# Kernel optimization log

Measured on AMD Instinct MI355X. Metric: run time of the kernel, lower is better.

The kernel has to match this reference:

```python
import jax, jax.numpy as jnp
import numpy as np

B, S, D, H = 2, 2048, 2048, 16
HD = D // H


def setup_inputs() -> dict:
    key = jax.random.key(0)
    ks = jax.random.split(key, 11)
    scale = 1.0 / np.sqrt(D)
    causal = jnp.tril(jnp.ones((S, S), dtype=bool))
    attention_mask = jnp.broadcast_to(causal, (B, H, S, S))
    return {
        "queries": jax.random.normal(ks[0], (B, S, D), dtype=jnp.float32),
        "keys": jax.random.normal(ks[1], (B, S, D), dtype=jnp.float32),
        "values": jax.random.normal(ks[2], (B, S, D), dtype=jnp.float32),
        "attention_mask": attention_mask,
        "wq": jax.random.normal(ks[3], (D, D), dtype=jnp.float32) * scale,
        "bq": jax.random.normal(ks[4], (D,), dtype=jnp.float32) * 0.01,
        "wk": jax.random.normal(ks[5], (D, D), dtype=jnp.float32) * scale,
        "bk": jax.random.normal(ks[6], (D,), dtype=jnp.float32) * 0.01,
        "wv": jax.random.normal(ks[7], (D, D), dtype=jnp.float32) * scale,
        "bv": jax.random.normal(ks[8], (D,), dtype=jnp.float32) * 0.01,
        "wo": jax.random.normal(ks[9], (D, D), dtype=jnp.float32) * scale,
        "bo": jax.random.normal(ks[10], (D,), dtype=jnp.float32) * 0.01,
    }


def _split_heads(x):
    # (B, S, D) -> (B, H, S, HD)
    b, s, _ = x.shape
    return x.reshape(b, s, H, HD).transpose(0, 2, 1, 3)


def reference(queries, keys, values, attention_mask, wq, bq, wk, bk, wv, bv, wo, bo):
    # Linear layers (torch convention: x @ W.T + b)
    q = _split_heads(queries @ wq.T + bq)   # (B, H, S, HD)
    k = _split_heads(keys @ wk.T + bk)
    v = _split_heads(values @ wv.T + bv)

    inv_sqrt_d = 1.0 / jnp.sqrt(jnp.asarray(HD, dtype=q.dtype))
    scores = jnp.einsum('bhqd,bhkd->bhqk', q, k) * inv_sqrt_d  # (B, H, S, S)
    scores = jnp.where(attention_mask, scores, jnp.asarray(-jnp.inf, dtype=scores.dtype))
    probs = jax.nn.softmax(scores, axis=-1)
    out = jnp.einsum('bhqk,bhkd->bhqd', probs, v)              # (B, H, S, HD)

    out = out.transpose(0, 2, 1, 3).reshape(queries.shape[0], queries.shape[1], D)
    return out @ wo.T + bo
```

## Files before the change

### kernel.cpp

```cpp
#include <hip/hip_runtime.h>
#include <hip/hip_bf16.h>

typedef unsigned short u16;
typedef __bf16 bf16x8 __attribute__((ext_vector_type(8)));
typedef short  short8 __attribute__((ext_vector_type(8)));
typedef float  f32x4  __attribute__((ext_vector_type(4)));
typedef u16    u16x4  __attribute__((ext_vector_type(4)));

#define BB 2
#define SS 2048
#define DD 2048
#define HH 16
#define HDIM 128
#define MM (BB * SS)
#define KSCALE 0.12752039505554602f

static __device__ __forceinline__ f32x4 mfma16(short8 a, short8 b, f32x4 c) {
    return __builtin_amdgcn_mfma_f32_16x16x32_bf16(
        __builtin_bit_cast(bf16x8, a), __builtin_bit_cast(bf16x8, b), c, 0, 0, 0);
}

static __device__ __forceinline__ u16 f2bf(float f) {
    union { float f; unsigned u; } v; v.f = f;
    unsigned r = v.u + 0x7fffu + ((v.u >> 16) & 1u);
    return (u16)(r >> 16);
}

static __device__ __forceinline__ float bf2f(u16 v) {
    union { unsigned u; float f; } t; t.u = ((unsigned)v) << 16;
    return t.f;
}

static __device__ __forceinline__ uint4 pack8(float4 a, float4 b) {
    uint4 o;
    o.x = (unsigned)f2bf(a.x) | ((unsigned)f2bf(a.y) << 16);
    o.y = (unsigned)f2bf(a.z) | ((unsigned)f2bf(a.w) << 16);
    o.z = (unsigned)f2bf(b.x) | ((unsigned)f2bf(b.y) << 16);
    o.w = (unsigned)f2bf(b.z) | ((unsigned)f2bf(b.w) << 16);
    return o;
}

static __device__ __forceinline__ void gload_lds16(const u16* g, u16* l) {
    __builtin_amdgcn_global_load_lds(
        (const __attribute__((address_space(1))) unsigned int*)g,
        (__attribute__((address_space(3))) unsigned int*)l, 16, 0, 0);
}

__global__ __launch_bounds__(256) void conv_all(
    const float* __restrict__ q, const float* __restrict__ k, const float* __restrict__ v,
    const float* __restrict__ wq, const float* __restrict__ wk,
    const float* __restrict__ wv, const float* __restrict__ wo,
    u16* __restrict__ out)
{
    constexpr int n1 = MM * DD / 8;
    constexpr int nw = DD * DD / 8;
    constexpr int total = 3 * n1 + 4 * nw;
    const int stride = gridDim.x * blockDim.x;
    for (int i = blockIdx.x * blockDim.x + threadIdx.x; i < total; i += stride) {
        const float* s; int j = i; float sc = 1.f;
        if (j < n1)            { s = q; }
        else if (j < 2 * n1)   { s = k;  j -= n1; }
        else if (j < 3 * n1)   { s = v;  j -= 2 * n1; }
        else {
            j -= 3 * n1;
            if (j < nw)        { s = wq; sc = KSCALE; }
            else if (j < 2*nw) { s = wk; j -= nw; }
            else if (j < 3*nw) { s = wv; j -= 2 * nw; }
            else               { s = wo; j -= 3 * nw; }
        }
        const float4* sp = (const float4*)s + (size_t)j * 2;
        float4 a = sp[0], bb2 = sp[1];
        a.x *= sc; a.y *= sc; a.z *= sc; a.w *= sc;
        bb2.x *= sc; bb2.y *= sc; bb2.z *= sc; bb2.w *= sc;
        ((uint4*)out)[i] = pack8(a, bb2);
    }
}

__global__ __launch_bounds__(256, 3) void gemm_qkv(
    const u16* __restrict__ A0, const u16* __restrict__ W0,
    const float* __restrict__ bq, const float* __restrict__ bk,
    const float* __restrict__ bv, u16* __restrict__ C0)
{
    __shared__ u16 S[128 * 132];
    u16* Al = S;
    u16* Bl = S + 4096;

    const int z = blockIdx.z;
    const u16* A  = A0 + (size_t)z * MM * DD;
    const u16* Wb = W0 + (size_t)z * DD * DD;
    const float* bias = (z == 0) ? bq : (z == 1 ? bk : bv);
    const float bsc = (z == 0) ? KSCALE : 1.f;

    const int tid = threadIdx.x;
    const int lane = tid & 63;
    const int lg = lane >> 4, li = lane & 15;
    const int wid = tid >> 6;
    const int brow = blockIdx.x * 128, bcol = blockIdx.y * 128;
    const int wm = wid >> 1, wn = wid & 1;

    const int srow = tid >> 2;
    const int scol = (tid & 3) * 8;

    const f32x4 zero = {0.f, 0.f, 0.f, 0.f};
    f32x4 acc[4][4];
#pragma unroll
    for (int i = 0; i < 4; ++i)
#pragma unroll
        for (int j = 0; j < 4; ++j) acc[i][j] = zero;

    const u16* aptr = A  + (size_t)(brow + srow) * DD + scol;
    const u16* bptr = Wb + (size_t)(bcol + srow) * DD + scol;
    const size_t half = (size_t)64 * DD;

    for (int kt = 0; kt < DD; kt += 32) {
        gload_lds16(aptr + kt,        &Al[tid * 8]);
        gload_lds16(aptr + half + kt, &Al[2048 + tid * 8]);
        gload_lds16(bptr + kt,        &Bl[tid * 8]);
        gload_lds16(bptr + half + kt, &Bl[2048 + tid * 8]);
        __syncthreads();

        short8 af[4], bf[4];
#pragma unroll
        for (int mi = 0; mi < 4; ++mi)
            af[mi] = *(const short8*)(&Al[(wm * 64 + mi * 16 + li) * 32 + lg * 8]);
#pragma unroll
        for (int ni = 0; ni < 4; ++ni)
            bf[ni] = *(const short8*)(&Bl[(wn * 64 + ni * 16 + li) * 32 + lg * 8]);
#pragma unroll
        for (int mi = 0; mi < 4; ++mi)
#pragma unroll
            for (int ni = 0; ni < 4; ++ni)
                acc[mi][ni] = mfma16(af[mi], bf[ni], acc[mi][ni]);
        __syncthreads();
    }

    if (z == 2) {
        u16* Cl = S;
#pragma unroll
        for (int ni = 0; ni < 4; ++ni) {
            const int cc = wn * 64 + ni * 16 + li;
            const float bvv = bias[bcol + cc];
#pragma unroll
            for (int mi = 0; mi < 4; ++mi)
#pragma unroll
                for (int r = 0; r < 4; ++r) {
                    const int rr = wm * 64 + mi * 16 + lg * 4 + r;
                    Cl[cc * 132 + rr] = f2bf(acc[mi][ni][r] + bvv);
                }
        }
        __syncthreads();
        const int row = tid >> 1;
        const int hcol = (tid & 1) * 64;
        u16* dst = C0 + (size_t)2 * MM * DD + (size_t)(bcol + row) * MM + brow + hcol;
#pragma unroll
        for (int c = 0; c < 8; ++c)
            *(short8*)(dst + c * 8) = *(const short8*)(&Cl[row * 132 + hcol + c * 8]);
    } else {
        u16* Cp = C0 + (size_t)z * MM * DD;
#pragma unroll
        for (int ni = 0; ni < 4; ++ni) {
            const int col = bcol + wn * 64 + ni * 16 + li;
            const float bvv = bias[col] * bsc;
#pragma unroll
            for (int mi = 0; mi < 4; ++mi)
#pragma unroll
                for (int r = 0; r < 4; ++r) {
                    const int row = brow + wm * 64 + mi * 16 + lg * 4 + r;
                    Cp[(size_t)row * DD + col] = f2bf(acc[mi][ni][r] + bvv);
                }
        }
    }
}

__global__ __launch_bounds__(256) void gemm_out(
    const u16* __restrict__ A, const u16* __restrict__ Wb,
    const float* __restrict__ bias, float* __restrict__ Cp)
{
    __shared__ u16 Al[128 * 32];
    __shared__ u16 Bl[128 * 32];

    const int tid = threadIdx.x;
    const int lane = tid & 63;
    const int lg = lane >> 4, li = lane & 15;
    const int wid = tid >> 6;
    const int brow = blockIdx.x * 128, bcol = blockIdx.y * 128;
    const int wm = wid >> 1, wn = wid & 1;

    const int srow = tid >> 2;
    const int scol = (tid & 3) * 8;

    const f32x4 zero = {0.f, 0.f, 0.f, 0.f};
    f32x4 acc[4][4];
#pragma unroll
    for (int i = 0; i < 4; ++i)
#pragma unroll
        for (int j = 0; j < 4; ++j) acc[i][j] = zero;

    const u16* aptr = A  + (size_t)(brow + srow) * DD + scol;
    const u16* bptr = Wb + (size_t)(bcol + srow) * DD + scol;
    const size_t half = (size_t)64 * DD;

    for (int kt = 0; kt < DD; kt += 32) {
        gload_lds16(aptr + kt,        &Al[tid * 8]);
        gload_lds16(aptr + half + kt, &Al[2048 + tid * 8]);
        gload_lds16(bptr + kt,        &Bl[tid * 8]);
        gload_lds16(bptr + half + kt, &Bl[2048 + tid * 8]);
        __syncthreads();

        short8 af[4], bf[4];
#pragma unroll
        for (int mi = 0; mi < 4; ++mi)
            af[mi] = *(const short8*)(&Al[(wm * 64 + mi * 16 + li) * 32 + lg * 8]);
#pragma unroll
        for (int ni = 0; ni < 4; ++ni)
            bf[ni] = *(const short8*)(&Bl[(wn * 64 + ni * 16 + li) * 32 + lg * 8]);
#pragma unroll
        for (int mi = 0; mi < 4; ++mi)
#pragma unroll
            for (int ni = 0; ni < 4; ++ni)
                acc[mi][ni] = mfma16(af[mi], bf[ni], acc[mi][ni]);
        __syncthreads();
    }

#pragma unroll
    for (int ni = 0; ni < 4; ++ni) {
        const int col = bcol + wn * 64 + ni * 16 + li;
        const float bvv = bias[col];
#pragma unroll
        for (int mi = 0; mi < 4; ++mi)
#pragma unroll
            for (int r = 0; r < 4; ++r) {
                const int row = brow + wm * 64 + mi * 16 + lg * 4 + r;
                Cp[(size_t)row * DD + col] = acc[mi][ni][r] + bvv;
            }
    }
}

__global__ __launch_bounds__(256) void flash_attn(
    const u16* __restrict__ Q, const u16* __restrict__ Kp,
    const u16* __restrict__ Vt, u16* __restrict__ O,
    u16* __restrict__ PartO, float* __restrict__ PartML)
{
    constexpr int SP = 72;
    __shared__ u16 lds[16384 + 4 * 32 * SP];
    u16* Kl = lds;
    u16* Vl = lds + 8192;
    u16* Pl = lds + 16384;

    const int tid = threadIdx.x;
    const int wid = tid >> 6, lane = tid & 63;
    const int lg = lane >> 4, li = lane & 15;
    const int h = blockIdx.y, b = blockIdx.z;

    const int f = 39 - (int)blockIdx.x;
    int qt, ch;
    if (f < 4)       { qt = f;               ch = 0; }
    else if (f < 12) { int g = f - 4;  qt = 4  + (g >> 1); ch = g & 1; }
    else if (f < 24) { int g = f - 12; qt = 8  + g / 3;    ch = g % 3; }
    else             { int g = f - 24; qt = 12 + (g >> 2); ch = g & 3; }
    const int j0 = ch * 8;
    const int j1 = min(j0 + 8, 2 * qt + 2);
    const int qbase = qt * 128 + wid * 32;

    const int rK0 = tid >> 4, wK0 = tid & 15;
    const int bK0 = ((wK0 * 16) ^ ((rK0 & 7) << 4)) >> 1;
    const int rV0 = tid >> 3, wV0 = tid & 7;
    const int bV0 = ((wV0 * 16) ^ ((rV0 & 7) << 4)) >> 1;
    const u16* kbase = Kp + (size_t)(b * SS + rK0) * DD + h * HDIM + bK0;
    const u16* vbase = Vt + (size_t)(h * HDIM + rV0) * MM + b * SS + bV0;

    short8 qf[4][2];
    {
        const u16* qp0 = Q + (size_t)(b * SS + qbase + li) * DD + h * HDIM + lg * 8;
#pragma unroll
        for (int qh = 0; qh < 2; ++qh)
#pragma unroll
            for (int s = 0; s < 4; ++s)
                qf[s][qh] = *(const short8*)(qp0 + (size_t)qh * 16 * DD + s * 32);
    }

    const f32x4 zero = {0.f, 0.f, 0.f, 0.f};
    float m_r[2], l_r[2];
    m_r[0] = m_r[1] = -__builtin_inff();
    l_r[0] = l_r[1] = 0.f;
    f32x4 accO[8][2];
#pragma unroll
    for (int d = 0; d < 8; ++d) accO[d][0] = accO[d][1] = zero;

    for (int j = j0; j < j1; ++j) {
#pragma unroll
        for (int i_ = 0; i_ < 4; ++i_) {
            gload_lds16(kbase + (size_t)(j * 64 + i_ * 16) * DD, &Kl[(i_ * 256 + tid) * 8]);
            gload_lds16(vbase + (size_t)(i_ * 32) * MM + j * 64, &Vl[(i_ * 256 + tid) * 8]);
        }
        __syncthreads();

        if (j * 64 <= qbase + 31) {
            f32x4 accS[4][2];
#pragma unroll
            for (int nb = 0; nb < 4; ++nb) accS[nb][0] = accS[nb][1] = zero;
            __builtin_amdgcn_s_setprio(1);
#pragma unroll
            for (int s = 0; s < 4; ++s) {
#pragma unroll
                for (int nb = 0; nb < 4; ++nb) {
                    const int R = nb * 16 + li;
                    const int e = ((s * 64 + lg * 16) ^ ((R & 7) << 4)) >> 1;
                    short8 kf = *(const short8*)(&Kl[R * 128 + e]);
#pragma unroll
                    for (int qh = 0; qh < 2; ++qh)
                        accS[nb][qh] = mfma16(kf, qf[s][qh], accS[nb][qh]);
                }
            }
            __builtin_amdgcn_s_setprio(0);

            const bool domask = (j * 64 + 63 > qbase);
            float rmax[2];
            rmax[0] = rmax[1] = -__builtin_inff();
#pragma unroll
            for (int nb = 0; nb < 4; ++nb)
#pragma unroll
                for (int qh = 0; qh < 2; ++qh)
#pragma unroll
                    for (int r = 0; r < 4; ++r) {
                        float t = accS[nb][qh][r];
                        if (domask && (j * 64 + nb * 16 + lg * 4 + r >
                                       qbase + qh * 16 + li)) t = -__builtin_inff();
                        accS[nb][qh][r] = t;
                        rmax[qh] = fmaxf(rmax[qh], t);
                    }
#pragma unroll
            for (int qh = 0; qh < 2; ++qh) {
                rmax[qh] = fmaxf(rmax[qh], __shfl_xor(rmax[qh], 16, 64));
                rmax[qh] = fmaxf(rmax[qh], __shfl_xor(rmax[qh], 32, 64));
            }

            const bool need = (rmax[0] - m_r[0] > 11.5f) || (rmax[1] - m_r[1] > 11.5f);
            if (__any(need)) {
#pragma unroll
                for (int qh = 0; qh < 2; ++qh) {
                    const float mn = fmaxf(m_r[qh], rmax[qh]);
                    const float sf = exp2f(m_r[qh] - mn);
                    m_r[qh] = mn;
                    l_r[qh] *= sf;
#pragma unroll
                    for (int mb = 0; mb < 8; ++mb)
#pragma unroll
                        for (int r = 0; r < 4; ++r) accO[mb][qh][r] *= sf;
                }
            }

            float ls[2] = {0.f, 0.f};
#pragma unroll
            for (int nb = 0; nb < 4; ++nb)
#pragma unroll
                for (int qh = 0; qh < 2; ++qh)
#pragma unroll
                    for (int r = 0; r < 4; ++r) {
                        const float e = exp2f(accS[nb][qh][r] - m_r[qh]);
                        accS[nb][qh][r] = e;
                        ls[qh] += e;
                    }
#pragma unroll
            for (int qh = 0; qh < 2; ++qh) {
                ls[qh] += __shfl_xor(ls[qh], 16, 64);
                ls[qh] += __shfl_xor(ls[qh], 32, 64);
                l_r[qh] += ls[qh];
            }

#pragma unroll
            for (int nb = 0; nb < 4; ++nb)
#pragma unroll
                for (int qh = 0; qh < 2; ++qh) {
                    u16x4 pk;
                    pk.x = f2bf(accS[nb][qh][0]);
                    pk.y = f2bf(accS[nb][qh][1]);
                    pk.z = f2bf(accS[nb][qh][2]);
                    pk.w = f2bf(accS[nb][qh][3]);
                    *(u16x4*)(&Pl[(wid * 32 + qh * 16 + li) * SP + nb * 16 + lg * 4]) = pk;
                }

            __builtin_amdgcn_s_setprio(1);
#pragma unroll
            for (int s2 = 0; s2 < 2; ++s2) {
                short8 pf[2];
#pragma unroll
                for (int qh = 0; qh < 2; ++qh)
                    pf[qh] = *(const short8*)(&Pl[(wid * 32 + qh * 16 + li) * SP +
                                                  s2 * 32 + lg * 8]);
#pragma unroll
                for (int mb = 0; mb < 8; ++mb) {
                    const int R2 = mb * 16 + li;
                    const int e2 = ((s2 * 64 + lg * 16) ^ ((R2 & 7) << 4)) >> 1;
                    short8 vf = *(const short8*)(&Vl[R2 * 64 + e2]);
#pragma unroll
                    for (int qh = 0; qh < 2; ++qh)
                        accO[mb][qh] = mfma16(vf, pf[qh], accO[mb][qh]);
                }
            }
            __builtin_amdgcn_s_setprio(0);
        }
        __syncthreads();
    }

    if (f >= 4) {
        const int pslot = (b * HH + h) * 36 + (f - 4);
        u16* po = PartO + (size_t)pslot * 16384;
#pragma unroll
        for (int mb = 0; mb < 8; ++mb)
#pragma unroll
            for (int qh = 0; qh < 2; ++qh) {
                const int q_g = wid * 32 + qh * 16 + li;
#pragma unroll
                for (int r = 0; r < 4; ++r) {
                    const int d = mb * 16 + lg * 4 + r;
                    po[d * 128 + q_g] = f2bf(accO[mb][qh][r]);
                }
            }
        if (lg == 0) {
            float* ml = PartML + (size_t)pslot * 256;
#pragma unroll
            for (int qh = 0; qh < 2; ++qh) {
                ml[wid * 32 + qh * 16 + li]       = m_r[qh];
                ml[128 + wid * 32 + qh * 16 + li] = l_r[qh];
            }
        }
    } else {
        float linv[2] = {1.f / l_r[0], 1.f / l_r[1]};
        u16* Wl = lds + wid * 4096;
#pragma unroll
        for (int mb = 0; mb < 8; ++mb)
#pragma unroll
            for (int qh = 0; qh < 2; ++qh) {
                const int q_l = qh * 16 + li;
                const int dbase = mb * 16 + lg * 4;
                u16x4 pk;
                pk.x = f2bf(accO[mb][qh][0] * linv[qh]);
                pk.y = f2bf(accO[mb][qh][1] * linv[qh]);
                pk.z = f2bf(accO[mb][qh][2] * linv[qh]);
                pk.w = f2bf(accO[mb][qh][3] * linv[qh]);
                *(u16x4*)(&Wl[q_l * 128 + (dbase ^ ((q_l & 7) << 4))]) = pk;
            }
        const int q_l = lane >> 1;
        const int d0 = (lane & 1) * 64;
        u16* op = O + (size_t)(b * SS + qt * 128 + wid * 32 + q_l) * DD + h * HDIM + d0;
#pragma unroll
        for (int c = 0; c < 8; ++c) {
            short8 vv = *(const short8*)(&Wl[q_l * 128 + ((d0 + c * 8) ^ ((q_l & 7) << 4))]);
            *(short8*)(op + c * 8) = vv;
        }
    }
}

__global__ __launch_bounds__(256) void attn_combine(
    const u16* __restrict__ PartO, const float* __restrict__ PartML,
    u16* __restrict__ O)
{
    const int qt = 4 + (int)blockIdx.x;
    const int h = blockIdx.y, b = blockIdx.z;
    const int nch = qt / 4 + 1;
    int f0m4;
    if (qt < 8)       f0m4 = (qt - 4) * 2;
    else if (qt < 12) f0m4 = 8 + (qt - 8) * 3;
    else              f0m4 = 20 + (qt - 12) * 4;
    const int pbase = (b * HH + h) * 36 + f0m4;

    const int tid = threadIdx.x;
    const int q = tid & 127;
    const int d0 = (tid >> 7) * 64;

    float mc[4], lc[4];
#pragma unroll
    for (int c = 0; c < 4; ++c) {
        if (c < nch) {
            mc[c] = PartML[(size_t)(pbase + c) * 256 + q];
            lc[c] = PartML[(size_t)(pbase + c) * 256 + 128 + q];
        } else { mc[c] = -__builtin_inff(); lc[c] = 0.f; }
    }
    float M = fmaxf(fmaxf(mc[0], mc[1]), fmaxf(mc[2], mc[3]));
    float wc[4], L = 0.f;
#pragma unroll
    for (int c = 0; c < 4; ++c) { wc[c] = exp2f(mc[c] - M); L += wc[c] * lc[c]; }
    const float Linv = 1.f / L;

    float acc[64];
#pragma unroll
    for (int i = 0; i < 64; ++i) acc[i] = 0.f;
#pragma unroll
    for (int c = 0; c < 4; ++c) {
        if (c < nch) {
            const float w = wc[c] * Linv;
            const u16* po = PartO + (size_t)(pbase + c) * 16384 + q;
#pragma unroll
            for (int i = 0; i < 64; ++i)
                acc[i] += w * bf2f(po[(size_t)(d0 + i) * 128]);
        }
    }

    u16* op = O + (size_t)(b * SS + qt * 128 + q) * DD + h * HDIM + d0;
#pragma unroll
    for (int j = 0; j < 8; ++j) {
        short8 vv;
#pragma unroll
        for (int e = 0; e < 8; ++e) vv[e] = (short)f2bf(acc[j * 8 + e]);
        *(short8*)(op + j * 8) = vv;
    }
}

extern "C" void kernel_launch(void* const* d_in, const int* in_sizes, int n_in,
                              void* d_out, int out_size, void* d_ws, size_t ws_size,
                              hipStream_t stream)
{
    const float* queries = (const float*)d_in[0];
    const float* keys    = (const float*)d_in[1];
    const float* values  = (const float*)d_in[2];
    const float* wq = (const float*)d_in[4];
    const float* bq = (const float*)d_in[5];
    const float* wk = (const float*)d_in[6];
    const float* bk = (const float*)d_in[7];
    const float* wv = (const float*)d_in[8];
    const float* bv = (const float*)d_in[9];
    const float* wo = (const float*)d_in[10];
    const float* bo = (const float*)d_in[11];

    const int NMD = MM * DD;
    const int NWW = DD * DD;

    u16* qb  = (u16*)d_ws;
    u16* wqb = qb  + (size_t)3 * NMD;
    u16* wob = wqb + (size_t)3 * NWW;
    u16* qw  = wob + (size_t)NWW;
    u16* aw  = qw  + (size_t)3 * NMD;
    u16*   partO  = qb;
    float* partML = (float*)wqb;
    (void)in_sizes; (void)n_in; (void)out_size; (void)ws_size;

    dim3 blk(256);
    dim3 gridC(2048);
    dim3 gridQKV(MM / 128, DD / 128, 3);
    dim3 gridO(MM / 128, DD / 128);
    dim3 gridA(40, HH, BB);
    dim3 gridX(12, HH, BB);

    conv_all<<<gridC, blk, 0, stream>>>(queries, keys, values, wq, wk, wv, wo, qb);
    gemm_qkv<<<gridQKV, blk, 0, stream>>>(qb, wqb, bq, bk, bv, qw);
    flash_attn<<<gridA, blk, 0, stream>>>(qw, qw + (size_t)NMD, qw + (size_t)2 * NMD, aw,
                                          partO, partML);
    attn_combine<<<gridX, blk, 0, stream>>>(partO, partML, aw);
    gemm_out<<<gridO, blk, 0, stream>>>(aw, wob, bo, (float*)d_out);
}
```

Measured before the change: 349.1 us.

## Switch flash attention to 32x32x16 MFMA with single-row-per-lane softmax

Rewrites the attention inner loops to use 32x32x16 bf16 MFMA instead of 16x16x32, so each lane owns a single query row. Row max and sum reductions need one cross-lane shuffle instead of two, fewer LDS fragment loads are issued per MFMA, and per-row softmax state shrinks to scalars. The partial-output layout changes from d-major to q-major so writes are vectorized, and the combine kernel reads contiguous elements to match. Risks include different register pressure, possible LDS bank conflicts from the new swizzle indexing, and correctness of the new C-fragment mapping.

```diff
diff --git a/kernel.cpp b/kernel.cpp
--- a/kernel.cpp
+++ b/kernel.cpp
@@ -5,6 +5,7 @@
 typedef __bf16 bf16x8 __attribute__((ext_vector_type(8)));
 typedef short  short8 __attribute__((ext_vector_type(8)));
 typedef float  f32x4  __attribute__((ext_vector_type(4)));
+typedef float  f32x16 __attribute__((ext_vector_type(16)));
 typedef u16    u16x4  __attribute__((ext_vector_type(4)));
 
 #define BB 2
@@ -17,6 +18,11 @@
 
 static __device__ __forceinline__ f32x4 mfma16(short8 a, short8 b, f32x4 c) {
     return __builtin_amdgcn_mfma_f32_16x16x32_bf16(
+        __builtin_bit_cast(bf16x8, a), __builtin_bit_cast(bf16x8, b), c, 0, 0, 0);
+}
+
+static __device__ __forceinline__ f32x16 mfma32(short8 a, short8 b, f32x16 c) {
+    return __builtin_amdgcn_mfma_f32_32x32x16_bf16(
         __builtin_bit_cast(bf16x8, a), __builtin_bit_cast(bf16x8, b), c, 0, 0, 0);
 }
 
@@ -249,7 +255,8 @@
 
     const int tid = threadIdx.x;
     const int wid = tid >> 6, lane = tid & 63;
-    const int lg = lane >> 4, li = lane & 15;
+    const int l5 = lane & 31;
+    const int hi = lane >> 5;
     const int h = blockIdx.y, b = blockIdx.z;
 
     const int f = 39 - (int)blockIdx.x;
@@ -261,6 +268,7 @@
     const int j0 = ch * 8;
     const int j1 = min(j0 + 8, 2 * qt + 2);
     const int qbase = qt * 128 + wid * 32;
+    const int qg = qbase + l5;
 
     const int rK0 = tid >> 4, wK0 = tid & 15;
     const int bK0 = ((wK0 * 16) ^ ((rK0 & 7) << 4)) >> 1;
@@ -269,23 +277,18 @@
     const u16* kbase = Kp + (size_t)(b * SS + rK0) * DD + h * HDIM + bK0;
     const u16* vbase = Vt + (size_t)(h * HDIM + rV0) * MM + b * SS + bV0;
 
-    short8 qf[4][2];
+    short8 qf[8];
     {
-        const u16* qp0 = Q + (size_t)(b * SS + qbase + li) * DD + h * HDIM + lg * 8;
-#pragma unroll
-        for (int qh = 0; qh < 2; ++qh)
-#pragma unroll
-            for (int s = 0; s < 4; ++s)
-                qf[s][qh] = *(const short8*)(qp0 + (size_t)qh * 16 * DD + s * 32);
-    }
-
-    const f32x4 zero = {0.f, 0.f, 0.f, 0.f};
-    float m_r[2], l_r[2];
-    m_r[0] = m_r[1] = -__builtin_inff();
-    l_r[0] = l_r[1] = 0.f;
-    f32x4 accO[8][2];
-#pragma unroll
-    for (int d = 0; d < 8; ++d) accO[d][0] = accO[d][1] = zero;
+        const u16* qp0 = Q + (size_t)(b * SS + qg) * DD + h * HDIM + hi * 8;
+#pragma unroll
+        for (int ks = 0; ks < 8; ++ks)
+            qf[ks] = *(const short8*)(qp0 + ks * 16);
+    }
+
+    float m_r = -__builtin_inff(), l_r = 0.f;
+    f32x16 accO[4];
+#pragma unroll
+    for (int d = 0; d < 4; ++d) accO[d] = (f32x16)(0.f);
 
     for (int j = j0; j < j1; ++j) {
 #pragma unroll
@@ -296,106 +299,78 @@
         __syncthreads();
 
         if (j * 64 <= qbase + 31) {
-            f32x4 accS[4][2];
-#pragma unroll
-            for (int nb = 0; nb < 4; ++nb) accS[nb][0] = accS[nb][1] = zero;
+            f32x16 accS[2];
+            accS[0] = (f32x16)(0.f); accS[1] = (f32x16)(0.f);
             __builtin_amdgcn_s_setprio(1);
 #pragma unroll
-            for (int s = 0; s < 4; ++s) {
-#pragma unroll
-                for (int nb = 0; nb < 4; ++nb) {
-                    const int R = nb * 16 + li;
-                    const int e = ((s * 64 + lg * 16) ^ ((R & 7) << 4)) >> 1;
-                    short8 kf = *(const short8*)(&Kl[R * 128 + e]);
-#pragma unroll
-                    for (int qh = 0; qh < 2; ++qh)
-                        accS[nb][qh] = mfma16(kf, qf[s][qh], accS[nb][qh]);
+            for (int ks = 0; ks < 8; ++ks) {
+#pragma unroll
+                for (int kvb = 0; kvb < 2; ++kvb) {
+                    const int row = kvb * 32 + l5;
+                    const int e = (ks * 16 + hi * 8) ^ ((row & 7) << 3);
+                    short8 kf = *(const short8*)(&Kl[row * 128 + e]);
+                    accS[kvb] = mfma32(kf, qf[ks], accS[kvb]);
                 }
             }
             __builtin_amdgcn_s_setprio(0);
 
             const bool domask = (j * 64 + 63 > qbase);
-            float rmax[2];
-            rmax[0] = rmax[1] = -__builtin_inff();
-#pragma unroll
-            for (int nb = 0; nb < 4; ++nb)
-#pragma unroll
-                for (int qh = 0; qh < 2; ++qh)
-#pragma unroll
-                    for (int r = 0; r < 4; ++r) {
-                        float t = accS[nb][qh][r];
-                        if (domask && (j * 64 + nb * 16 + lg * 4 + r >
-                                       qbase + qh * 16 + li)) t = -__builtin_inff();
-                        accS[nb][qh][r] = t;
-                        rmax[qh] = fmaxf(rmax[qh], t);
-                    }
-#pragma unroll
-            for (int qh = 0; qh < 2; ++qh) {
-                rmax[qh] = fmaxf(rmax[qh], __shfl_xor(rmax[qh], 16, 64));
-                rmax[qh] = fmaxf(rmax[qh], __shfl_xor(rmax[qh], 32, 64));
+            float rmax = -__builtin_inff();
+#pragma unroll
+            for (int kvb = 0; kvb < 2; ++kvb)
+#pragma unroll
+                for (int r = 0; r < 16; ++r) {
+                    float t = accS[kvb][r];
+                    const int kv = j * 64 + kvb * 32 + (r & 3) + 8 * (r >> 2) + 4 * hi;
+                    if (domask && kv > qg) t = -__builtin_inff();
+                    accS[kvb][r] = t;
+                    rmax = fmaxf(rmax, t);
+                }
+            rmax = fmaxf(rmax, __shfl_xor(rmax, 32, 64));
+
+            if (!__all(rmax - m_r <= 11.5f)) {
+                const float mn = fmaxf(m_r, rmax);
+                const float sf = exp2f(m_r - mn);
+                m_r = mn;
+                l_r *= sf;
+#pragma unroll
+                for (int db = 0; db < 4; ++db) accO[db] = accO[db] * sf;
             }
 
-            const bool need = (rmax[0] - m_r[0] > 11.5f) || (rmax[1] - m_r[1] > 11.5f);
-            if (__any(need)) {
-#pragma unroll
-                for (int qh = 0; qh < 2; ++qh) {
-                    const float mn = fmaxf(m_r[qh], rmax[qh]);
-                    const float sf = exp2f(m_r[qh] - mn);
-                    m_r[qh] = mn;
-                    l_r[qh] *= sf;
-#pragma unroll
-                    for (int mb = 0; mb < 8; ++mb)
-#pragma unroll
-                        for (int r = 0; r < 4; ++r) accO[mb][qh][r] *= sf;
-                }
-            }
-
-            float ls[2] = {0.f, 0.f};
-#pragma unroll
-            for (int nb = 0; nb < 4; ++nb)
-#pragma unroll
-                for (int qh = 0; qh < 2; ++qh)
-#pragma unroll
-                    for (int r = 0; r < 4; ++r) {
-                        const float e = exp2f(accS[nb][qh][r] - m_r[qh]);
-                        accS[nb][qh][r] = e;
-                        ls[qh] += e;
-                    }
-#pragma unroll
-            for (int qh = 0; qh < 2; ++qh) {
-                ls[qh] += __shfl_xor(ls[qh], 16, 64);
-                ls[qh] += __shfl_xor(ls[qh], 32, 64);
-                l_r[qh] += ls[qh];
-            }
-
-#pragma unroll
-            for (int nb = 0; nb < 4; ++nb)
-#pragma unroll
-                for (int qh = 0; qh < 2; ++qh) {
+            float ls = 0.f;
+#pragma unroll
+            for (int kvb = 0; kvb < 2; ++kvb)
+#pragma unroll
+                for (int r = 0; r < 16; ++r) {
+                    const float e = exp2f(accS[kvb][r] - m_r);
+                    accS[kvb][r] = e;
+                    ls += e;
+                }
+            ls += __shfl_xor(ls, 32, 64);
+            l_r += ls;
+
+#pragma unroll
+            for (int kvb = 0; kvb < 2; ++kvb)
+#pragma unroll
+                for (int g = 0; g < 4; ++g) {
                     u16x4 pk;
-                    pk.x = f2bf(accS[nb][qh][0]);
-                    pk.y = f2bf(accS[nb][qh][1]);
-                    pk.z = f2bf(accS[nb][qh][2]);
-                    pk.w = f2bf(accS[nb][qh][3]);
-                    *(u16x4*)(&Pl[(wid * 32 + qh * 16 + li) * SP + nb * 16 + lg * 4]) = pk;
+                    pk.x = f2bf(accS[kvb][g * 4 + 0]);
+                    pk.y = f2bf(accS[kvb][g * 4 + 1]);
+                    pk.z = f2bf(accS[kvb][g * 4 + 2]);
+                    pk.w = f2bf(accS[kvb][g * 4 + 3]);
+                    *(u16x4*)(&Pl[(wid * 32 + l5) * SP + kvb * 32 + g * 8 + hi * 4]) = pk;
                 }
 
             __builtin_amdgcn_s_setprio(1);
 #pragma unroll
-            for (int s2 = 0; s2 < 2; ++s2) {
-                short8 pf[2];
-#pragma unroll
-                for (int qh = 0; qh < 2; ++qh)
-                    pf[qh] = *(const short8*)(&Pl[(wid * 32 + qh * 16 + li) * SP +
-                                                  s2 * 32 + lg * 8]);
-#pragma unroll
-                for (int mb = 0; mb < 8; ++mb) {
-                    const int R2 = mb * 16 + li;
-                    const int e2 = ((s2 * 64 + lg * 16) ^ ((R2 & 7) << 4)) >> 1;
-                    short8 vf = *(const short8*)(&Vl[R2 * 64 + e2]);
-#pragma unroll
-                    for (int qh = 0; qh < 2; ++qh)
-                        accO[mb][qh] = mfma16(vf, pf[qh], accO[mb][qh]);
+            for (int ks = 0; ks < 4; ++ks) {
+                short8 pf = *(const short8*)(&Pl[(wid * 32 + l5) * SP + ks * 16 + hi * 8]);
+#pragma unroll
+                for (int db = 0; db < 4; ++db) {
+                    const int row = db * 32 + l5;
+                    const int e = (ks * 16 + hi * 8) ^ ((row & 7) << 3);
+                    short8 vf = *(const short8*)(&Vl[row * 64 + e]);
+                    accO[db] = mfma32(vf, pf, accO[db]);
                 }
             }
             __builtin_amdgcn_s_setprio(0);
@@ -405,48 +380,45 @@
 
     if (f >= 4) {
         const int pslot = (b * HH + h) * 36 + (f - 4);
-        u16* po = PartO + (size_t)pslot * 16384;
-#pragma unroll
-        for (int mb = 0; mb < 8; ++mb)
-#pragma unroll
-            for (int qh = 0; qh < 2; ++qh) {
-                const int q_g = wid * 32 + qh * 16 + li;
-#pragma unroll
-                for (int r = 0; r < 4; ++r) {
-                    const int d = mb * 16 + lg * 4 + r;
-                    po[d * 128 + q_g] = f2bf(accO[mb][qh][r]);
-                }
+        u16* po = PartO + (size_t)pslot * 16384 + (size_t)(wid * 32 + l5) * 128;
+#pragma unroll
+        for (int db = 0; db < 4; ++db)
+#pragma unroll
+            for (int g = 0; g < 4; ++g) {
+                const int d0 = db * 32 + g * 8 + hi * 4;
+                u16x4 pk;
+                pk.x = f2bf(accO[db][g * 4 + 0]);
+                pk.y = f2bf(accO[db][g * 4 + 1]);
+                pk.z = f2bf(accO[db][g * 4 + 2]);
+                pk.w = f2bf(accO[db][g * 4 + 3]);
+                *(u16x4*)(po + d0) = pk;
             }
-        if (lg == 0) {
+        if (lane < 32) {
             float* ml = PartML + (size_t)pslot * 256;
-#pragma unroll
-            for (int qh = 0; qh < 2; ++qh) {
-                ml[wid * 32 + qh * 16 + li]       = m_r[qh];
-                ml[128 + wid * 32 + qh * 16 + li] = l_r[qh];
-            }
+            ml[wid * 32 + l5]       = m_r;
+            ml[128 + wid * 32 + l5] = l_r;
         }
     } else {
-        float linv[2] = {1.f / l_r[0], 1.f / l_r[1]};
+        const float linv = 1.f / l_r;
         u16* Wl = lds + wid * 4096;
 #pragma unroll
-        for (int mb = 0; mb < 8; ++mb)
-#pragma unroll
-            for (int qh = 0; qh < 2; ++qh) {
-                const int q_l = qh * 16 + li;
-                const int dbase = mb * 16 + lg * 4;
+        for (int db = 0; db < 4; ++db)
+#pragma unroll
+            for (int g = 0; g < 4; ++g) {
+                const int d0 = db * 32 + g * 8 + hi * 4;
                 u16x4 pk;
-                pk.x = f2bf(accO[mb][qh][0] * linv[qh]);
-                pk.y = f2bf(accO[mb][qh][1] * linv[qh]);
-                pk.z = f2bf(accO[mb][qh][2] * linv[qh]);
-                pk.w = f2bf(accO[mb][qh][3] * linv[qh]);
-                *(u16x4*)(&Wl[q_l * 128 + (dbase ^ ((q_l & 7) << 4))]) = pk;
+                pk.x = f2bf(accO[db][g * 4 + 0] * linv);
+                pk.y = f2bf(accO[db][g * 4 + 1] * linv);
+                pk.z = f2bf(accO[db][g * 4 + 2] * linv);
+                pk.w = f2bf(accO[db][g * 4 + 3] * linv);
+                *(u16x4*)(&Wl[l5 * 128 + (d0 ^ ((l5 & 7) << 4))]) = pk;
             }
         const int q_l = lane >> 1;
-        const int d0 = (lane & 1) * 64;
-        u16* op = O + (size_t)(b * SS + qt * 128 + wid * 32 + q_l) * DD + h * HDIM + d0;
+        const int d0r = (lane & 1) * 64;
+        u16* op = O + (size_t)(b * SS + qt * 128 + wid * 32 + q_l) * DD + h * HDIM + d0r;
 #pragma unroll
         for (int c = 0; c < 8; ++c) {
-            short8 vv = *(const short8*)(&Wl[q_l * 128 + ((d0 + c * 8) ^ ((q_l & 7) << 4))]);
+            short8 vv = *(const short8*)(&Wl[q_l * 128 + ((d0r + c * 8) ^ ((q_l & 7) << 4))]);
             *(short8*)(op + c * 8) = vv;
         }
     }
@@ -490,10 +462,10 @@
     for (int c = 0; c < 4; ++c) {
         if (c < nch) {
             const float w = wc[c] * Linv;
-            const u16* po = PartO + (size_t)(pbase + c) * 16384 + q;
+            const u16* po = PartO + (size_t)(pbase + c) * 16384 + (size_t)q * 128 + d0;
 #pragma unroll
             for (int i = 0; i < 64; ++i)
-                acc[i] += w * bf2f(po[(size_t)(d0 + i) * 128]);
+                acc[i] += w * bf2f(po[i]);
         }
     }
 
```

After: 350.8 us. No clear change (+0.5%).
